# Kernel tuning notes

Measured on AMD Instinct MI355X. Metric: run time of the kernel, lower is better.

Reference implementation:

```python
import jax, jax.numpy as jnp
import numpy as np

D_MODEL = 256
NUM_HEADS = 8
NUM_KV_HEADS = 4
HEAD_DIM = D_MODEL // NUM_HEADS
EPS = 1e-5


def layer_norm(x, g, b):
    mu = jnp.mean(x, axis=-1, keepdims=True)
    var = jnp.var(x, axis=-1, keepdims=True)
    return (x - mu) * jax.lax.rsqrt(var + EPS) * g + b


def gqa(x_q, x_kv, Wq, bq, Wk, bk, Wv, bv, Wo, bo):
    # x_q, x_kv: [BC, S, D]
    BC, S, D = x_q.shape
    G = NUM_HEADS // NUM_KV_HEADS
    q = (x_q @ Wq + bq).reshape(BC, S, NUM_HEADS, HEAD_DIM)
    k = (x_kv @ Wk + bk).reshape(BC, S, NUM_KV_HEADS, HEAD_DIM)
    v = (x_kv @ Wv + bv).reshape(BC, S, NUM_KV_HEADS, HEAD_DIM)
    # repeat_interleave over head dim to expand KV heads to query heads
    k = jnp.repeat(k, G, axis=2)
    v = jnp.repeat(v, G, axis=2)
    scale = 1.0 / np.sqrt(HEAD_DIM).astype(np.float32)
    scores = jnp.einsum('bqhd,bkhd->bhqk', q, k) * scale  # [BC,H,S,S]
    attn = jax.nn.softmax(scores, axis=-1)
    out = jnp.einsum('bhqk,bkhd->bqhd', attn, v).reshape(BC, S, D)
    return out @ Wo + bo


def _make_params(key):
    ks = jax.random.split(key, 20)
    D, Dkv = D_MODEL, NUM_KV_HEADS * HEAD_DIM
    s = 1.0 / np.sqrt(D).astype(np.float32)
    p = {}
    # 4 LayerNorms
    for name in ['spec_q', 'spec_kv', 'spat_q', 'spat_kv']:
        p[f'ln_{name}_g'] = jnp.ones((D,), jnp.float32)
        p[f'ln_{name}_b'] = jnp.zeros((D,), jnp.float32)
    # two GQA modules: s2t and t2s
    i = 0
    for tag in ['s2t', 't2s']:
        p[f'Wq_{tag}'] = jax.random.normal(ks[i], (D, D), jnp.float32) * s; i += 1
        p[f'bq_{tag}'] = jnp.zeros((D,), jnp.float32)
        p[f'Wk_{tag}'] = jax.random.normal(ks[i], (D, Dkv), jnp.float32) * s; i += 1
        p[f'bk_{tag}'] = jnp.zeros((Dkv,), jnp.float32)
        p[f'Wv_{tag}'] = jax.random.normal(ks[i], (D, Dkv), jnp.float32) * s; i += 1
        p[f'bv_{tag}'] = jnp.zeros((Dkv,), jnp.float32)
        p[f'Wo_{tag}'] = jax.random.normal(ks[i], (D, D), jnp.float32) * s; i += 1
        p[f'bo_{tag}'] = jnp.zeros((D,), jnp.float32)
    p['gate_spec'] = jnp.zeros((1,), jnp.float32)
    p['gate_spat'] = jnp.zeros((1,), jnp.float32)
    return p


def setup_inputs() -> dict:
    key = jax.random.key(0)
    k1, k2, k3 = jax.random.split(key, 3)
    B, S, C, D = 8, 64, 128, D_MODEL
    inp = {
        'x_spec': jax.random.normal(k1, (B, S, C, D), jnp.float32),
        'x_spat': jax.random.normal(k2, (B, S, C, D), jnp.float32),
    }
    inp.update(_make_params(k3))
    return inp


def reference(x_spec, x_spat,
              ln_spec_q_g, ln_spec_q_b, ln_spec_kv_g, ln_spec_kv_b,
              ln_spat_q_g, ln_spat_q_b, ln_spat_kv_g, ln_spat_kv_b,
              Wq_s2t, bq_s2t, Wk_s2t, bk_s2t, Wv_s2t, bv_s2t, Wo_s2t, bo_s2t,
              Wq_t2s, bq_t2s, Wk_t2s, bk_t2s, Wv_t2s, bv_t2s, Wo_t2s, bo_t2s,
              gate_spec, gate_spat):
    B, S, C, D = x_spec.shape
    # (B,S,C,D) -> (B*C, S, D)
    spec_flat = jnp.transpose(x_spec, (0, 2, 1, 3)).reshape(B * C, S, D)
    spat_flat = jnp.transpose(x_spat, (0, 2, 1, 3)).reshape(B * C, S, D)

    spec_q = layer_norm(spec_flat, ln_spec_q_g, ln_spec_q_b)
    spat_kv = layer_norm(spat_flat, ln_spat_kv_g, ln_spat_kv_b)
    delta_spec = gqa(spec_q, spat_kv, Wq_s2t, bq_s2t, Wk_s2t, bk_s2t, Wv_s2t, bv_s2t, Wo_s2t, bo_s2t)

    spat_q = layer_norm(spat_flat, ln_spat_q_g, ln_spat_q_b)
    spec_kv = layer_norm(spec_flat, ln_spec_kv_g, ln_spec_kv_b)
    delta_spat = gqa(spat_q, spec_kv, Wq_t2s, bq_t2s, Wk_t2s, bk_t2s, Wv_t2s, bv_t2s, Wo_t2s, bo_t2s)

    delta_spec = jnp.transpose(delta_spec.reshape(B, C, S, D), (0, 2, 1, 3))
    delta_spat = jnp.transpose(delta_spat.reshape(B, C, S, D), (0, 2, 1, 3))

    out_spec = x_spec + jax.nn.sigmoid(gate_spec) * delta_spec
    out_spat = x_spat + jax.nn.sigmoid(gate_spat) * delta_spat
    return (out_spec, out_spat)
```

## Files before the change

kernel.cpp:

```cpp
#include <hip/hip_runtime.h>

typedef short short8 __attribute__((ext_vector_type(8)));
typedef float f32x4 __attribute__((ext_vector_type(4)));

#define NELT 16777216

__device__ __forceinline__ float b2f(unsigned short u) {
    return __uint_as_float(((unsigned)u) << 16);
}
__device__ __forceinline__ unsigned short f2b(float f) {
    unsigned u = __float_as_uint(f);
    u += 0x7FFF + ((u >> 16) & 1);
    return (unsigned short)(u >> 16);
}
__device__ __forceinline__ void split2(float f, unsigned short& hi, unsigned short& lo) {
    unsigned short h = f2b(f);
    hi = h;
    lo = f2b(f - b2f(h));
}
__device__ __forceinline__ int xrow_off(int r) {
    int n = r >> 6, s = r & 63;
    int b = n >> 7, c = n & 127;
    return (((b << 6) + s) * 128 + c) << 8;
}
__device__ __forceinline__ int sw256(int row, int k) {
    return row * 256 + ((((k >> 3) ^ (row & 7)) << 3) | (k & 7));
}
__device__ __forceinline__ int boff(int nt, int kk, int ct, int lq, int lm) {
    return ((((nt * 8 + kk) * 4 + ct) * 4 + lq) * 16 + lm) * 16;
}

struct WArgs {
    const float* Wq[2]; const float* Wk[2]; const float* Wv[2]; const float* Wo[2];
    unsigned short* Bqkv[2]; unsigned short* Bo[2];
};
__global__ __launch_bounds__(256) void w_prep(WArgs A)
{
    const int dir = blockIdx.y;
    const int tid = blockIdx.x * 256 + threadIdx.x;
    const int lm = tid & 15, lq = (tid >> 4) & 3, ct = (tid >> 6) & 3;
    const int kk = (tid >> 8) & 7, nt = tid >> 11;
    const int c = ct * 16 + lm;
    {
        const float* W; int ldw, col;
        if (nt < 4)      { W = A.Wq[dir]; ldw = 256; col = nt * 64 + c; }
        else if (nt < 6) { W = A.Wk[dir]; ldw = 128; col = (nt - 4) * 64 + c; }
        else             { W = A.Wv[dir]; ldw = 128; col = (nt - 6) * 64 + c; }
        short8 h8, l8;
        #pragma unroll
        for (int j = 0; j < 8; ++j) {
            int k = kk * 32 + lq * 8 + j;
            unsigned short h, l;
            split2(W[k * ldw + col], h, l);
            h8[j] = (short)h; l8[j] = (short)l;
        }
        int off = boff(nt, kk, ct, lq, lm);
        *(short8*)&A.Bqkv[dir][off] = h8;
        *(short8*)&A.Bqkv[dir][off + 8] = l8;
    }
    if (nt < 4) {
        int col = nt * 64 + c;
        short8 h8, l8;
        #pragma unroll
        for (int j = 0; j < 8; ++j) {
            int k = kk * 32 + lq * 8 + j;
            unsigned short h, l;
            split2(A.Wo[dir][k * 256 + col], h, l);
            h8[j] = (short)h; l8[j] = (short)l;
        }
        int off = boff(nt, kk, ct, lq, lm);
        *(short8*)&A.Bo[dir][off] = h8;
        *(short8*)&A.Bo[dir][off + 8] = l8;
    }
}

struct FusedArgs {
    const float* xq[2];   const float* xkv[2];
    const float* gq[2];   const float* btq[2];
    const float* gkv[2];  const float* btkv[2];
    const unsigned short* Bqkv[2];
    const unsigned short* Bow[2];
    const float* bq[2];   const float* bk[2];
    const float* bv[2];   const float* bo[2];
    const float* gate[2];
    float* out[2];
};

__global__ __launch_bounds__(512, 4) void fused(FusedArgs P_)
{
    __shared__ char SM[65536];
    unsigned short* Ah = (unsigned short*)SM;
    unsigned short* Al = (unsigned short*)(SM + 32768);
    const int dir = blockIdx.y;
    const int n = blockIdx.x, t = threadIdx.x;
    const int r0 = n * 64;
    const int w = t >> 6, l = t & 63, lm = l & 15, lq = l >> 4;

    const float* xq  = P_.xq[dir];
    const float* xkv = P_.xkv[dir];
    const unsigned short* Bq  = P_.Bqkv[dir];
    const unsigned short* BoW = P_.Bow[dir];

    auto stage = [&](const float* X, const float4& gv, const float4& b4) {
        #pragma unroll
        for (int half = 0; half < 2; ++half) {
            float4 xv[4];
            #pragma unroll
            for (int it = 0; it < 4; ++it)
                xv[it] = *(const float4*)(X + xrow_off(r0 + (half * 4 + it) * 8 + w) + l * 4);
            #pragma unroll
            for (int it = 0; it < 4; ++it) {
                int row = (half * 4 + it) * 8 + w;
                float4 x4 = xv[it];
                float s1 = x4.x + x4.y + x4.z + x4.w;
                float s2 = x4.x * x4.x + x4.y * x4.y + x4.z * x4.z + x4.w * x4.w;
                #pragma unroll
                for (int m = 1; m < 64; m <<= 1) {
                    s1 += __shfl_xor(s1, m);
                    s2 += __shfl_xor(s2, m);
                }
                float mu = s1 * (1.f / 256.f);
                float rstd = rsqrtf(s2 * (1.f / 256.f) - mu * mu + 1e-5f);
                float v0 = (x4.x - mu) * rstd * gv.x + b4.x;
                float v1 = (x4.y - mu) * rstd * gv.y + b4.y;
                float v2 = (x4.z - mu) * rstd * gv.z + b4.z;
                float v3 = (x4.w - mu) * rstd * gv.w + b4.w;
                ushort4 oh, ol;
                split2(v0, oh.x, ol.x); split2(v1, oh.y, ol.y);
                split2(v2, oh.z, ol.z); split2(v3, oh.w, ol.w);
                *(ushort4*)&Ah[sw256(row, l * 4)] = oh;
                *(ushort4*)&Al[sw256(row, l * 4)] = ol;
            }
        }
    };
    auto gemm32 = [&](f32x4 (&acc)[4][2], const unsigned short* B,
                      int nt, int ct0) {
        #pragma unroll
        for (int kk = 0; kk < 8; ++kk) {
            int k0 = kk * 32 + lq * 8;
            short8 bh[2], bl[2];
            #pragma unroll
            for (int i = 0; i < 2; ++i) {
                int off = boff(nt, kk, ct0 + i, lq, lm);
                bh[i] = *(const short8*)&B[off];
                bl[i] = *(const short8*)&B[off + 8];
            }
            #pragma unroll
            for (int m = 0; m < 4; ++m) {
                short8 ah = *(const short8*)&Ah[sw256(m * 16 + lm, k0)];
                short8 al = *(const short8*)&Al[sw256(m * 16 + lm, k0)];
                #pragma unroll
                for (int i = 0; i < 2; ++i) {
                    acc[m][i] = __builtin_amdgcn_mfma_f32_16x16x32_bf16(ah, bh[i], acc[m][i], 0, 0, 0);
                    acc[m][i] = __builtin_amdgcn_mfma_f32_16x16x32_bf16(al, bh[i], acc[m][i], 0, 0, 0);
                    acc[m][i] = __builtin_amdgcn_mfma_f32_16x16x32_bf16(ah, bl[i], acc[m][i], 0, 0, 0);
                }
            }
        }
    };

    {
        const float4 gv = *(const float4*)(P_.gkv[dir] + l * 4);
        const float4 b4 = *(const float4*)(P_.btkv[dir] + l * 4);
        stage(xkv, gv, b4);
    }
    __syncthreads();
    {
        f32x4 acc[4][2] = {};
        const int wk = w & 3;
        const bool isV = w >= 4;
        const int nt = (isV ? 6 : 4) + (wk >> 1);
        const int ct0 = (wk & 1) * 2;
        gemm32(acc, Bq, nt, ct0);
        __syncthreads();
        const float* bias = isV ? P_.bv[dir] : P_.bk[dir];
        float bi0 = bias[wk * 32 + lm], bi1 = bias[wk * 32 + 16 + lm];
        if (!isV) {
            unsigned short* Ks = (unsigned short*)(SM + wk * 5120);
            #pragma unroll
            for (int m = 0; m < 4; ++m)
                #pragma unroll
                for (int rg = 0; rg < 4; ++rg) {
                    int key = m * 16 + lq * 4 + rg;
                    Ks[key * 40 + lm]      = f2b(acc[m][0][rg] + bi0);
                    Ks[key * 40 + 16 + lm] = f2b(acc[m][1][rg] + bi1);
                }
        } else {
            unsigned short* Vs = (unsigned short*)(SM + 20480 + wk * 4608);
            #pragma unroll
            for (int m = 0; m < 4; ++m)
                #pragma unroll
                for (int rg = 0; rg < 4; ++rg) {
                    int key = m * 16 + lq * 4 + rg;
                    Vs[lm * 72 + key]        = f2b(acc[m][0][rg] + bi0);
                    Vs[(16 + lm) * 72 + key] = f2b(acc[m][1][rg] + bi1);
                }
        }
    }
    __syncthreads();

    const int g2 = w >> 1;
    short8 kf[4];
    {
        const unsigned short* Ks = (const unsigned short*)(SM + g2 * 5120);
        #pragma unroll
        for (int nt = 0; nt < 4; ++nt)
            kf[nt] = *(const short8*)&Ks[(nt * 16 + lm) * 40 + lq * 8];
    }
    short8 vb[2][2];
    {
        const unsigned short* Vs = (const unsigned short*)(SM + 20480 + g2 * 4608);
        #pragma unroll
        for (int kt = 0; kt < 2; ++kt) {
            vb[kt][0] = *(const short8*)&Vs[lm * 72 + kt * 32 + lq * 8];
            vb[kt][1] = *(const short8*)&Vs[(16 + lm) * 72 + kt * 32 + lq * 8];
        }
    }
    __syncthreads();

    {
        const float4 gv = *(const float4*)(P_.gq[dir] + l * 4);
        const float4 b4 = *(const float4*)(P_.btq[dir] + l * 4);
        stage(xq, gv, b4);
    }
    __syncthreads();
    f32x4 o[4][2] = {};
    {
        f32x4 qacc[4][2] = {};
        gemm32(qacc, Bq, w >> 1, (w & 1) * 2);
        __syncthreads();
        unsigned short* Qs = (unsigned short*)(SM + w * 5120);
        float bq0 = P_.bq[dir][w * 32 + lm], bq1 = P_.bq[dir][w * 32 + 16 + lm];
        #pragma unroll
        for (int m = 0; m < 4; ++m)
            #pragma unroll
            for (int rg = 0; rg < 4; ++rg) {
                int row = (m * 16 + lq * 4 + rg) * 40;
                Qs[row + lm]      = f2b(qacc[m][0][rg] + bq0);
                Qs[row + 16 + lm] = f2b(qacc[m][1][rg] + bq1);
            }
        unsigned short* Ps = (unsigned short*)(SM + 40960 + w * 2304);
        const float scale = 0.17677669529663687f;
        #pragma unroll 1
        for (int mt = 0; mt < 4; ++mt) {
            short8 qf = *(const short8*)&Qs[(mt * 16 + lm) * 40 + lq * 8];
            f32x4 s[4];
            #pragma unroll
            for (int nt = 0; nt < 4; ++nt) {
                f32x4 z = {0, 0, 0, 0};
                s[nt] = __builtin_amdgcn_mfma_f32_16x16x32_bf16(qf, kf[nt], z, 0, 0, 0);
            }
            #pragma unroll
            for (int rg = 0; rg < 4; ++rg) {
                float mx = fmaxf(fmaxf(s[0][rg], s[1][rg]),
                                 fmaxf(s[2][rg], s[3][rg]));
                #pragma unroll
                for (int msk = 1; msk < 16; msk <<= 1)
                    mx = fmaxf(mx, __shfl_xor(mx, msk));
                float p0 = __expf((s[0][rg] - mx) * scale);
                float p1 = __expf((s[1][rg] - mx) * scale);
                float p2 = __expf((s[2][rg] - mx) * scale);
                float p3 = __expf((s[3][rg] - mx) * scale);
                float sum = p0 + p1 + p2 + p3;
                #pragma unroll
                for (int msk = 1; msk < 16; msk <<= 1)
                    sum += __shfl_xor(sum, msk);
                float inv = 1.f / sum;
                int rowb = (lq * 4 + rg) * 72 + lm;
                Ps[rowb + 0]  = f2b(p0 * inv);
                Ps[rowb + 16] = f2b(p1 * inv);
                Ps[rowb + 32] = f2b(p2 * inv);
                Ps[rowb + 48] = f2b(p3 * inv);
            }
            #pragma unroll
            for (int kt = 0; kt < 2; ++kt) {
                short8 pa = *(const short8*)&Ps[lm * 72 + kt * 32 + lq * 8];
                o[mt][0] = __builtin_amdgcn_mfma_f32_16x16x32_bf16(pa, vb[kt][0], o[mt][0], 0, 0, 0);
                o[mt][1] = __builtin_amdgcn_mfma_f32_16x16x32_bf16(pa, vb[kt][1], o[mt][1], 0, 0, 0);
            }
        }
    }
    __syncthreads();

    #pragma unroll
    for (int m = 0; m < 4; ++m)
        #pragma unroll
        for (int n2 = 0; n2 < 2; ++n2)
            #pragma unroll
            for (int rg = 0; rg < 4; ++rg) {
                int row = m * 16 + lq * 4 + rg;
                int col = w * 32 + n2 * 16 + lm;
                unsigned short h_, l_;
                split2(o[m][n2][rg], h_, l_);
                int sw = sw256(row, col);
                Ah[sw] = h_;
                Al[sw] = l_;
            }
    __syncthreads();
    {
        f32x4 acc[4][2] = {};
        gemm32(acc, BoW, w >> 1, (w & 1) * 2);
        float sig = 1.f / (1.f + __expf(-P_.gate[dir][0]));
        const float* Xres = xq;
        float* Out = P_.out[dir];
        #pragma unroll
        for (int i = 0; i < 2; ++i) {
            int col = w * 32 + i * 16 + lm;
            float bias = P_.bo[dir][col];
            #pragma unroll
            for (int m = 0; m < 4; ++m)
                #pragma unroll
                for (int rg = 0; rg < 4; ++rg) {
                    int row = m * 16 + lq * 4 + rg;
                    int oidx = xrow_off(r0 + row) + col;
                    Out[oidx] = Xres[oidx] + sig * (acc[m][i][rg] + bias);
                }
        }
    }
}

extern "C" void kernel_launch(void* const* d_in, const int* in_sizes, int n_in,
                              void* d_out, int out_size, void* d_ws, size_t ws_size,
                              hipStream_t stream) {
    const float* x_spec = (const float*)d_in[0];
    const float* x_spat = (const float*)d_in[1];
    const float* ln_g[4] = {(const float*)d_in[2], (const float*)d_in[4],
                            (const float*)d_in[6], (const float*)d_in[8]};
    const float* ln_b[4] = {(const float*)d_in[3], (const float*)d_in[5],
                            (const float*)d_in[7], (const float*)d_in[9]};
    char* ws = (char*)d_ws;
    unsigned short* Bqkv[2] = {(unsigned short*)ws,
                               (unsigned short*)(ws + (512 << 10))};
    unsigned short* BoL[2]  = {(unsigned short*)(ws + (1024 << 10)),
                               (unsigned short*)(ws + (1280 << 10))};

    WArgs WA;
    for (int dir = 0; dir < 2; ++dir) {
        int base = 10 + dir * 8;
        WA.Wq[dir] = (const float*)d_in[base + 0];
        WA.Wk[dir] = (const float*)d_in[base + 2];
        WA.Wv[dir] = (const float*)d_in[base + 4];
        WA.Wo[dir] = (const float*)d_in[base + 6];
        WA.Bqkv[dir] = Bqkv[dir];
        WA.Bo[dir]   = BoL[dir];
    }
    w_prep<<<dim3(64, 2), 256, 0, stream>>>(WA);

    FusedArgs A;
    for (int dir = 0; dir < 2; ++dir) {
        int base = 10 + dir * 8;
        A.xq[dir]   = dir == 0 ? x_spec : x_spat;
        A.xkv[dir]  = dir == 0 ? x_spat : x_spec;
        A.gq[dir]   = dir == 0 ? ln_g[0] : ln_g[2];
        A.btq[dir]  = dir == 0 ? ln_b[0] : ln_b[2];
        A.gkv[dir]  = dir == 0 ? ln_g[3] : ln_g[1];
        A.btkv[dir] = dir == 0 ? ln_b[3] : ln_b[1];
        A.Bqkv[dir] = Bqkv[dir];
        A.Bow[dir]  = BoL[dir];
        A.bq[dir]   = (const float*)d_in[base + 1];
        A.bk[dir]   = (const float*)d_in[base + 3];
        A.bv[dir]   = (const float*)d_in[base + 5];
        A.bo[dir]   = (const float*)d_in[base + 7];
        A.gate[dir] = (const float*)d_in[26 + dir];
        A.out[dir]  = (float*)d_out + (size_t)dir * NELT;
    }
    fused<<<dim3(1024, 2), 512, 0, stream>>>(A);
}
```

Measured before the change: 507.4 us.

## Stage LayerNorm and GEMM operands in 32-row halves with a rearranged LDS map

The kernel now normalizes and stages 32 rows at a time into a half-size hi/lo bf16 A buffer and runs each projection GEMM in two halves. The out-projection input is split and staged the same way. K/V/P buffers move to a separate LDS region and the Q row stride shrinks, giving a 70 KB LDS footprint instead of 64 KB. The intent is to reshape the LDS plan and interleave staging with MFMA work. The cost is extra block-wide barriers and a larger total allocation, which could limit how many blocks fit on a CU.

```diff
diff --git a/kernel.cpp b/kernel.cpp
--- a/kernel.cpp
+++ b/kernel.cpp
@@ -88,9 +88,9 @@
 
 __global__ __launch_bounds__(512, 4) void fused(FusedArgs P_)
 {
-    __shared__ char SM[65536];
+    __shared__ char SM[71680];
     unsigned short* Ah = (unsigned short*)SM;
-    unsigned short* Al = (unsigned short*)(SM + 32768);
+    unsigned short* Al = (unsigned short*)(SM + 16384);
     const int dir = blockIdx.y;
     const int n = blockIdx.x, t = threadIdx.x;
     const int r0 = n * 64;
@@ -101,40 +101,37 @@
     const unsigned short* Bq  = P_.Bqkv[dir];
     const unsigned short* BoW = P_.Bow[dir];
 
-    auto stage = [&](const float* X, const float4& gv, const float4& b4) {
-        #pragma unroll
-        for (int half = 0; half < 2; ++half) {
-            float4 xv[4];
-            #pragma unroll
-            for (int it = 0; it < 4; ++it)
-                xv[it] = *(const float4*)(X + xrow_off(r0 + (half * 4 + it) * 8 + w) + l * 4);
-            #pragma unroll
-            for (int it = 0; it < 4; ++it) {
-                int row = (half * 4 + it) * 8 + w;
-                float4 x4 = xv[it];
-                float s1 = x4.x + x4.y + x4.z + x4.w;
-                float s2 = x4.x * x4.x + x4.y * x4.y + x4.z * x4.z + x4.w * x4.w;
-                #pragma unroll
-                for (int m = 1; m < 64; m <<= 1) {
-                    s1 += __shfl_xor(s1, m);
-                    s2 += __shfl_xor(s2, m);
-                }
-                float mu = s1 * (1.f / 256.f);
-                float rstd = rsqrtf(s2 * (1.f / 256.f) - mu * mu + 1e-5f);
-                float v0 = (x4.x - mu) * rstd * gv.x + b4.x;
-                float v1 = (x4.y - mu) * rstd * gv.y + b4.y;
-                float v2 = (x4.z - mu) * rstd * gv.z + b4.z;
-                float v3 = (x4.w - mu) * rstd * gv.w + b4.w;
-                ushort4 oh, ol;
-                split2(v0, oh.x, ol.x); split2(v1, oh.y, ol.y);
-                split2(v2, oh.z, ol.z); split2(v3, oh.w, ol.w);
-                *(ushort4*)&Ah[sw256(row, l * 4)] = oh;
-                *(ushort4*)&Al[sw256(row, l * 4)] = ol;
-            }
+    auto stage_half = [&](const float* X, const float4& gv, const float4& b4, int h) {
+        float4 xv[4];
+        #pragma unroll
+        for (int it = 0; it < 4; ++it)
+            xv[it] = *(const float4*)(X + xrow_off(r0 + h * 32 + it * 8 + w) + l * 4);
+        #pragma unroll
+        for (int it = 0; it < 4; ++it) {
+            int row = it * 8 + w;
+            float4 x4 = xv[it];
+            float s1 = x4.x + x4.y + x4.z + x4.w;
+            float s2 = x4.x * x4.x + x4.y * x4.y + x4.z * x4.z + x4.w * x4.w;
+            #pragma unroll
+            for (int m = 1; m < 64; m <<= 1) {
+                s1 += __shfl_xor(s1, m);
+                s2 += __shfl_xor(s2, m);
+            }
+            float mu = s1 * (1.f / 256.f);
+            float rstd = rsqrtf(s2 * (1.f / 256.f) - mu * mu + 1e-5f);
+            float v0 = (x4.x - mu) * rstd * gv.x + b4.x;
+            float v1 = (x4.y - mu) * rstd * gv.y + b4.y;
+            float v2 = (x4.z - mu) * rstd * gv.z + b4.z;
+            float v3 = (x4.w - mu) * rstd * gv.w + b4.w;
+            ushort4 oh, ol;
+            split2(v0, oh.x, ol.x); split2(v1, oh.y, ol.y);
+            split2(v2, oh.z, ol.z); split2(v3, oh.w, ol.w);
+            *(ushort4*)&Ah[sw256(row, l * 4)] = oh;
+            *(ushort4*)&Al[sw256(row, l * 4)] = ol;
         }
     };
-    auto gemm32 = [&](f32x4 (&acc)[4][2], const unsigned short* B,
-                      int nt, int ct0) {
+    auto gemm_half = [&](f32x4 (&acc)[4][2], const unsigned short* B,
+                         int nt, int ct0, int h) {
         #pragma unroll
         for (int kk = 0; kk < 8; ++kk) {
             int k0 = kk * 32 + lq * 8;
@@ -146,9 +143,10 @@
                 bl[i] = *(const short8*)&B[off + 8];
             }
             #pragma unroll
-            for (int m = 0; m < 4; ++m) {
-                short8 ah = *(const short8*)&Ah[sw256(m * 16 + lm, k0)];
-                short8 al = *(const short8*)&Al[sw256(m * 16 + lm, k0)];
+            for (int m2 = 0; m2 < 2; ++m2) {
+                short8 ah = *(const short8*)&Ah[sw256(m2 * 16 + lm, k0)];
+                short8 al = *(const short8*)&Al[sw256(m2 * 16 + lm, k0)];
+                int m = 2 * h + m2;
                 #pragma unroll
                 for (int i = 0; i < 2; ++i) {
                     acc[m][i] = __builtin_amdgcn_mfma_f32_16x16x32_bf16(ah, bh[i], acc[m][i], 0, 0, 0);
@@ -162,21 +160,22 @@
     {
         const float4 gv = *(const float4*)(P_.gkv[dir] + l * 4);
         const float4 b4 = *(const float4*)(P_.btkv[dir] + l * 4);
-        stage(xkv, gv, b4);
-    }
-    __syncthreads();
-    {
         f32x4 acc[4][2] = {};
         const int wk = w & 3;
         const bool isV = w >= 4;
         const int nt = (isV ? 6 : 4) + (wk >> 1);
         const int ct0 = (wk & 1) * 2;
-        gemm32(acc, Bq, nt, ct0);
-        __syncthreads();
+        #pragma unroll
+        for (int h = 0; h < 2; ++h) {
+            stage_half(xkv, gv, b4, h);
+            __syncthreads();
+            gemm_half(acc, Bq, nt, ct0, h);
+            __syncthreads();
+        }
         const float* bias = isV ? P_.bv[dir] : P_.bk[dir];
         float bi0 = bias[wk * 32 + lm], bi1 = bias[wk * 32 + 16 + lm];
         if (!isV) {
-            unsigned short* Ks = (unsigned short*)(SM + wk * 5120);
+            unsigned short* Ks = (unsigned short*)(SM + 32768 + wk * 5120);
             #pragma unroll
             for (int m = 0; m < 4; ++m)
                 #pragma unroll
@@ -186,7 +185,7 @@
                     Ks[key * 40 + 16 + lm] = f2b(acc[m][1][rg] + bi1);
                 }
         } else {
-            unsigned short* Vs = (unsigned short*)(SM + 20480 + wk * 4608);
+            unsigned short* Vs = (unsigned short*)(SM + 53248 + wk * 4608);
             #pragma unroll
             for (int m = 0; m < 4; ++m)
                 #pragma unroll
@@ -197,53 +196,52 @@
                 }
         }
     }
-    __syncthreads();
-
-    const int g2 = w >> 1;
-    short8 kf[4];
-    {
-        const unsigned short* Ks = (const unsigned short*)(SM + g2 * 5120);
-        #pragma unroll
-        for (int nt = 0; nt < 4; ++nt)
-            kf[nt] = *(const short8*)&Ks[(nt * 16 + lm) * 40 + lq * 8];
-    }
-    short8 vb[2][2];
-    {
-        const unsigned short* Vs = (const unsigned short*)(SM + 20480 + g2 * 4608);
-        #pragma unroll
-        for (int kt = 0; kt < 2; ++kt) {
-            vb[kt][0] = *(const short8*)&Vs[lm * 72 + kt * 32 + lq * 8];
-            vb[kt][1] = *(const short8*)&Vs[(16 + lm) * 72 + kt * 32 + lq * 8];
-        }
-    }
-    __syncthreads();
-
+
+    f32x4 o[4][2] = {};
     {
         const float4 gv = *(const float4*)(P_.gq[dir] + l * 4);
         const float4 b4 = *(const float4*)(P_.btq[dir] + l * 4);
-        stage(xq, gv, b4);
-    }
-    __syncthreads();
-    f32x4 o[4][2] = {};
-    {
         f32x4 qacc[4][2] = {};
-        gemm32(qacc, Bq, w >> 1, (w & 1) * 2);
-        __syncthreads();
-        unsigned short* Qs = (unsigned short*)(SM + w * 5120);
+        #pragma unroll
+        for (int h = 0; h < 2; ++h) {
+            stage_half(xq, gv, b4, h);
+            __syncthreads();
+            gemm_half(qacc, Bq, w >> 1, (w & 1) * 2, h);
+            __syncthreads();
+        }
+        unsigned short* Qs = (unsigned short*)(SM + w * 4096);
         float bq0 = P_.bq[dir][w * 32 + lm], bq1 = P_.bq[dir][w * 32 + 16 + lm];
         #pragma unroll
         for (int m = 0; m < 4; ++m)
             #pragma unroll
             for (int rg = 0; rg < 4; ++rg) {
-                int row = (m * 16 + lq * 4 + rg) * 40;
+                int row = (m * 16 + lq * 4 + rg) * 32;
                 Qs[row + lm]      = f2b(qacc[m][0][rg] + bq0);
                 Qs[row + 16 + lm] = f2b(qacc[m][1][rg] + bq1);
             }
-        unsigned short* Ps = (unsigned short*)(SM + 40960 + w * 2304);
+        const int g2 = w >> 1;
+        short8 kf[4];
+        {
+            const unsigned short* Ks = (const unsigned short*)(SM + 32768 + g2 * 5120);
+            #pragma unroll
+            for (int nt = 0; nt < 4; ++nt)
+                kf[nt] = *(const short8*)&Ks[(nt * 16 + lm) * 40 + lq * 8];
+        }
+        __syncthreads();
+        short8 vb[2][2];
+        {
+            const unsigned short* Vs = (const unsigned short*)(SM + 53248 + g2 * 4608);
+            #pragma unroll
+            for (int kt = 0; kt < 2; ++kt) {
+                vb[kt][0] = *(const short8*)&Vs[lm * 72 + kt * 32 + lq * 8];
+                vb[kt][1] = *(const short8*)&Vs[(16 + lm) * 72 + kt * 32 + lq * 8];
+            }
+        }
+        unsigned short* Ps = (unsigned short*)(SM + 32768 + w * 2304);
         const float scale = 0.17677669529663687f;
         #pragma unroll 1
         for (int mt = 0; mt < 4; ++mt) {
-            short8 qf = *(const short8*)&Qs[(mt * 16 + lm) * 40 + lq * 8];
+            short8 qf = *(const short8*)&Qs[(mt * 16 + lm) * 32 + lq * 8];
             f32x4 s[4];
             #pragma unroll
             for (int nt = 0; nt < 4; ++nt) {
@@ -282,24 +280,30 @@
     }
     __syncthreads();
 
-    #pragma unroll
-    for (int m = 0; m < 4; ++m)
-        #pragma unroll
-        for (int n2 = 0; n2 < 2; ++n2)
-            #pragma unroll
-            for (int rg = 0; rg < 4; ++rg) {
-                int row = m * 16 + lq * 4 + rg;
-                int col = w * 32 + n2 * 16 + lm;
-                unsigned short h_, l_;
-                split2(o[m][n2][rg], h_, l_);
-                int sw = sw256(row, col);
-                Ah[sw] = h_;
-                Al[sw] = l_;
-            }
-    __syncthreads();
     {
         f32x4 acc[4][2] = {};
-        gemm32(acc, BoW, w >> 1, (w & 1) * 2);
+        #pragma unroll
+        for (int h = 0; h < 2; ++h) {
+            #pragma unroll
+            for (int m2 = 0; m2 < 2; ++m2) {
+                int mt = 2 * h + m2;
+                #pragma unroll
+                for (int n2 = 0; n2 < 2; ++n2)
+                    #pragma unroll
+                    for (int rg = 0; rg < 4; ++rg) {
+                        int row = m2 * 16 + lq * 4 + rg;
+                        int col = w * 32 + n2 * 16 + lm;
+                        unsigned short h_, l_;
+                        split2(o[mt][n2][rg], h_, l_);
+                        int sw = sw256(row, col);
+                        Ah[sw] = h_;
+                        Al[sw] = l_;
+                    }
+            }
+            __syncthreads();
+            gemm_half(acc, BoW, w >> 1, (w & 1) * 2, h);
+            __syncthreads();
+        }
         float sig = 1.f / (1.f + __expf(-P_.gate[dir][0]));
         const float* Xres = xq;
         float* Out = P_.out[dir];
```

New measurement: 473.3 us. -6.7%, faster.
